# Performance work log

Measured on AMD Instinct MI355X. Metric: run time of the kernel, lower is better.

## Reference

```python
import jax, jax.numpy as jnp
import numpy as np


def setup_inputs() -> dict:
    key = jax.random.key(0)
    k1, k2, k3 = jax.random.split(key, 3)
    B, N, D = 4, 4096, 1024
    x = jax.random.normal(k1, (B, N, D), dtype=jnp.float32)
    # torch nn.Linear default init ~ U(-1/sqrt(D), 1/sqrt(D)); scale normals similarly
    scale = 1.0 / np.sqrt(D)
    Wq = jax.random.normal(k2, (D, D), dtype=jnp.float32) * scale
    Wk = jax.random.normal(k3, (D, D), dtype=jnp.float32) * scale
    return {"x": x, "Wq": Wq, "Wk": Wk}


def reference(x, Wq, Wk):
    # torch Linear: y = x @ W.T (weight shape [out, in])
    D = x.shape[-1]
    q = jnp.einsum('bnd,ed->bne', x, Wq)  # [B,N,D]
    k = jnp.einsum('bnd,ed->bne', x, Wk)  # [B,N,D]
    scores = jnp.einsum('bqd,bkd->bqk', q, k) / jnp.sqrt(jnp.float32(D))
    attn = jax.nn.softmax(scores, axis=-1)  # [B,N,N]
    return jnp.einsum('bqk,bkd->bqd', attn, x)
```

## Files before the change

### kernel.cpp

```cpp
#include <hip/hip_runtime.h>
#include <stdint.h>
#include <math.h>

typedef __attribute__((ext_vector_type(8))) short short8;
typedef __attribute__((ext_vector_type(4))) float fx4;
typedef unsigned int u32;

#define MFMA16(a, b, c) __builtin_amdgcn_mfma_f32_16x16x32_bf16(a, b, c, 0, 0, 0)
#define SCL 0.04508422002777948f

__device__ __forceinline__ unsigned short f2bfu(float f) {
  unsigned u = __builtin_bit_cast(unsigned, f);
  u += 0x7fffu + ((u >> 16) & 1u);
  return (unsigned short)(u >> 16);
}

__device__ __forceinline__ void gl_lds16(const void* g, void* l) {
  __builtin_amdgcn_global_load_lds(
      (const __attribute__((address_space(1))) u32*)g,
      (__attribute__((address_space(3))) u32*)l, 16, 0, 0);
}

__global__ __launch_bounds__(256) void prep_kernel(const float* __restrict__ x,
                                                   unsigned short* __restrict__ xT,
                                                   unsigned short* __restrict__ xbf) {
  __shared__ float tile[64 * 65];
  const int b = blockIdx.z, n0 = blockIdx.x * 64, d0 = blockIdx.y * 64;
  const int tid = threadIdx.x;
  const float* xb = x + ((size_t)b * 4096 + n0) * 1024 + d0;
#pragma unroll
  for (int i = 0; i < 4; i++) {
    int idx = tid + 256 * i;
    int r = idx >> 4, c4 = (idx & 15) * 4;
    const float4 v = *(const float4*)(xb + (size_t)r * 1024 + c4);
    float* tp = &tile[r * 65 + c4];
    tp[0] = v.x; tp[1] = v.y; tp[2] = v.z; tp[3] = v.w;
    uint2 pkt;
    pkt.x = (u32)f2bfu(v.x) | ((u32)f2bfu(v.y) << 16);
    pkt.y = (u32)f2bfu(v.z) | ((u32)f2bfu(v.w) << 16);
    *(uint2*)(xbf + ((size_t)b * 4096 + n0 + r) * 1024 + d0 + c4) = pkt;
  }
  __syncthreads();
  unsigned short* xo = xT + ((size_t)b * 1024 + d0) * 4096 + n0;
#pragma unroll
  for (int i = 0; i < 4; i++) {
    int idx = tid + 256 * i;
    int dr = idx >> 4, n4 = (idx & 15) * 4;
    unsigned short h0 = f2bfu(tile[(n4 + 0) * 65 + dr]);
    unsigned short h1 = f2bfu(tile[(n4 + 1) * 65 + dr]);
    unsigned short h2 = f2bfu(tile[(n4 + 2) * 65 + dr]);
    unsigned short h3 = f2bfu(tile[(n4 + 3) * 65 + dr]);
    uint2 pkt;
    pkt.x = (u32)h0 | ((u32)h1 << 16);
    pkt.y = (u32)h2 | ((u32)h3 << 16);
    *(uint2*)(xo + (size_t)dr * 4096 + n4) = pkt;
  }
}

__global__ __launch_bounds__(256) void wconv_kernel(const float* __restrict__ Wq,
                                                    const float* __restrict__ Wk,
                                                    unsigned short* __restrict__ Wqb,
                                                    unsigned short* __restrict__ Wkb) {
  int gid = blockIdx.x * 256 + threadIdx.x;
  const float* s = (gid < 262144) ? Wq : Wk;
  unsigned short* d = (gid < 262144) ? Wqb : Wkb;
  int off = (gid & 262143) * 4;
  const float4 v = *(const float4*)(s + off);
  uint2 pkt;
  pkt.x = (u32)f2bfu(v.x) | ((u32)f2bfu(v.y) << 16);
  pkt.y = (u32)f2bfu(v.z) | ((u32)f2bfu(v.w) << 16);
  *(uint2*)(d + off) = pkt;
}


__global__ __launch_bounds__(256) void proj_kernel(
    const unsigned short* __restrict__ xbf, const unsigned short* __restrict__ Wqb,
    const unsigned short* __restrict__ Wkb, unsigned short* __restrict__ Qo,
    unsigned short* __restrict__ Ko) {
  const unsigned short* Wb = blockIdx.z ? Wkb : Wqb;
  unsigned short* O = blockIdx.z ? Ko : Qo;
  __shared__ __attribute__((aligned(16))) short Als[128 * 64];
  __shared__ __attribute__((aligned(16))) short Bls[128 * 64];
  const int m0 = blockIdx.x * 128, e0 = blockIdx.y * 128;
  const int tid = threadIdx.x;
  const int wave = tid >> 6, lane = tid & 63;
  const int wm = wave & 1, wn = wave >> 1;
  const int quad = lane >> 4, l16 = lane & 15;

  const unsigned short* ag[4];
  const unsigned short* bg[4];
  short* al[4];
  short* bl[4];
#pragma unroll
  for (int i = 0; i < 4; i++) {
    const int s = tid + 256 * i;
    const int row = s >> 3, o = (s & 7) ^ (row & 7);
    ag[i] = xbf + (size_t)(m0 + row) * 1024 + o * 8;
    bg[i] = Wb + (size_t)(e0 + row) * 1024 + o * 8;
    al[i] = Als + s * 8;
    bl[i] = Bls + s * 8;
  }
  int aoff[4][2], boff[4][2];
#pragma unroll
  for (int t = 0; t < 4; t++)
#pragma unroll
    for (int st = 0; st < 2; st++) {
      const int ra = 64 * wm + 16 * t + l16;
      const int rb = 64 * wn + 16 * t + l16;
      aoff[t][st] = ra * 64 + (((st * 4 + quad) ^ (ra & 7)) * 8);
      boff[t][st] = rb * 64 + (((st * 4 + quad) ^ (rb & 7)) * 8);
    }

  fx4 acc[4][4];
#pragma unroll
  for (int i = 0; i < 4; i++)
#pragma unroll
    for (int j = 0; j < 4; j++) acc[i][j] = (fx4)0.f;

  for (int k0 = 0; k0 < 1024; k0 += 64) {
#pragma unroll
    for (int i = 0; i < 4; i++) {
      gl_lds16(ag[i] + k0, al[i]);
      gl_lds16(bg[i] + k0, bl[i]);
    }
    __syncthreads();
#pragma unroll
    for (int st = 0; st < 2; st++) {
      short8 af[4], bfv[4];
#pragma unroll
      for (int t = 0; t < 4; t++) {
        af[t] = *(const short8*)&Als[aoff[t][st]];
        bfv[t] = *(const short8*)&Bls[boff[t][st]];
      }
#pragma unroll
      for (int mt = 0; mt < 4; mt++)
#pragma unroll
        for (int nt = 0; nt < 4; nt++)
          acc[mt][nt] = MFMA16(af[mt], bfv[nt], acc[mt][nt]);
    }
    __syncthreads();
  }
#pragma unroll
  for (int mt = 0; mt < 4; mt++) {
    const int row = m0 + 64 * wm + 16 * mt + 4 * quad;
#pragma unroll
    for (int nt = 0; nt < 4; nt++) {
      const int col = e0 + 64 * wn + 16 * nt + l16;
      unsigned short* op = O + (size_t)row * 1024 + col;
#pragma unroll
      for (int i = 0; i < 4; i++) op[(size_t)i * 1024] = f2bfu(acc[mt][nt][i]);
    }
  }
}

__global__ __launch_bounds__(256) void qk_kernel(
    const unsigned short* __restrict__ Qb, const unsigned short* __restrict__ Kb,
    unsigned short* __restrict__ P, int bbase) {
  const int bz = blockIdx.z, b = bbase + bz;
  const unsigned short* A = Qb + (size_t)b * 4096 * 1024;
  const unsigned short* B = Kb + (size_t)b * 4096 * 1024;
  unsigned short* Pb = P + (size_t)bz * 4096 * 4096;
  __shared__ __attribute__((aligned(16))) short Als[128 * 64];
  __shared__ __attribute__((aligned(16))) short Bls[128 * 64];
  const int m0 = blockIdx.x * 128, n0 = blockIdx.y * 128;
  const int tid = threadIdx.x;
  const int wave = tid >> 6, lane = tid & 63;
  const int wm = wave & 1, wn = wave >> 1;
  const int quad = lane >> 4, l16 = lane & 15;

  const unsigned short* ag[4];
  const unsigned short* bg[4];
  short* al[4];
  short* bl[4];
#pragma unroll
  for (int i = 0; i < 4; i++) {
    const int s = tid + 256 * i;
    const int row = s >> 3, o = (s & 7) ^ (row & 7);
    ag[i] = A + (size_t)(m0 + row) * 1024 + o * 8;
    bg[i] = B + (size_t)(n0 + row) * 1024 + o * 8;
    al[i] = Als + s * 8;
    bl[i] = Bls + s * 8;
  }
  int aoff[4][2], boff[4][2];
#pragma unroll
  for (int t = 0; t < 4; t++)
#pragma unroll
    for (int st = 0; st < 2; st++) {
      const int ra = 64 * wm + 16 * t + l16;
      const int rb = 64 * wn + 16 * t + l16;
      aoff[t][st] = ra * 64 + (((st * 4 + quad) ^ (ra & 7)) * 8);
      boff[t][st] = rb * 64 + (((st * 4 + quad) ^ (rb & 7)) * 8);
    }

  fx4 acc[4][4];
#pragma unroll
  for (int i = 0; i < 4; i++)
#pragma unroll
    for (int j = 0; j < 4; j++) acc[i][j] = (fx4)0.f;

  for (int k0 = 0; k0 < 1024; k0 += 64) {
#pragma unroll
    for (int i = 0; i < 4; i++) {
      gl_lds16(ag[i] + k0, al[i]);
      gl_lds16(bg[i] + k0, bl[i]);
    }
    __syncthreads();
#pragma unroll
    for (int st = 0; st < 2; st++) {
      short8 af[4], bfv[4];
#pragma unroll
      for (int t = 0; t < 4; t++) {
        af[t] = *(const short8*)&Als[aoff[t][st]];
        bfv[t] = *(const short8*)&Bls[boff[t][st]];
      }
#pragma unroll
      for (int mt = 0; mt < 4; mt++)
#pragma unroll
        for (int nt = 0; nt < 4; nt++)
          acc[mt][nt] = MFMA16(af[mt], bfv[nt], acc[mt][nt]);
    }
    __syncthreads();
  }
#pragma unroll
  for (int mt = 0; mt < 4; mt++) {
    const int row = m0 + 64 * wm + 16 * mt + 4 * quad;
#pragma unroll
    for (int nt = 0; nt < 4; nt++) {
      const int col = n0 + 64 * wn + 16 * nt + l16;
      unsigned short* pp = Pb + (size_t)row * 4096 + col;
#pragma unroll
      for (int i = 0; i < 4; i++)
        pp[(size_t)i * 4096] = f2bfu(exp2f(acc[mt][nt][i] * SCL));
    }
  }
}

__global__ __launch_bounds__(256) void pv_kernel(
    const unsigned short* __restrict__ P, const unsigned short* __restrict__ xT,
    unsigned short* __restrict__ Ost, int bbase) {
  const int bz = blockIdx.z, b = bbase + bz;
  const unsigned short* A = P + (size_t)bz * 4096 * 4096;
  const unsigned short* B = xT + (size_t)b * 1024 * 4096;
  unsigned short* O = Ost + (size_t)b * 4096 * 1024;
  __shared__ __attribute__((aligned(16))) short Als[128 * 64];
  __shared__ __attribute__((aligned(16))) short Bls[128 * 64];
  const int m0 = blockIdx.x * 128, e0 = blockIdx.y * 128;
  const int tid = threadIdx.x;
  const int wave = tid >> 6, lane = tid & 63;
  const int wm = wave & 1, wn = wave >> 1;
  const int quad = lane >> 4, l16 = lane & 15;

  const unsigned short* ag[4];
  const unsigned short* bg[4];
  short* al[4];
  short* bl[4];
#pragma unroll
  for (int i = 0; i < 4; i++) {
    const int s = tid + 256 * i;
    const int row = s >> 3, o = (s & 7) ^ (row & 7);
    ag[i] = A + (size_t)(m0 + row) * 4096 + o * 8;
    bg[i] = B + (size_t)(e0 + row) * 4096 + o * 8;
    al[i] = Als + s * 8;
    bl[i] = Bls + s * 8;
  }
  int aoff[4][2], boff[4][2];
#pragma unroll
  for (int t = 0; t < 4; t++)
#pragma unroll
    for (int st = 0; st < 2; st++) {
      const int ra = 64 * wm + 16 * t + l16;
      const int rb = 64 * wn + 16 * t + l16;
      aoff[t][st] = ra * 64 + (((st * 4 + quad) ^ (ra & 7)) * 8);
      boff[t][st] = rb * 64 + (((st * 4 + quad) ^ (rb & 7)) * 8);
    }

  short8 ones;
#pragma unroll
  for (int i = 0; i < 8; i++) ones[i] = (short)0x3F80;

  fx4 acc[4][4], accl[4];
#pragma unroll
  for (int i = 0; i < 4; i++) {
    accl[i] = (fx4)0.f;
#pragma unroll
    for (int j = 0; j < 4; j++) acc[i][j] = (fx4)0.f;
  }

  for (int k0 = 0; k0 < 4096; k0 += 64) {
#pragma unroll
    for (int i = 0; i < 4; i++) {
      gl_lds16(ag[i] + k0, al[i]);
      gl_lds16(bg[i] + k0, bl[i]);
    }
    __syncthreads();
#pragma unroll
    for (int st = 0; st < 2; st++) {
      short8 af[4], bfv[4];
#pragma unroll
      for (int t = 0; t < 4; t++) {
        af[t] = *(const short8*)&Als[aoff[t][st]];
        bfv[t] = *(const short8*)&Bls[boff[t][st]];
      }
#pragma unroll
      for (int mt = 0; mt < 4; mt++) {
#pragma unroll
        for (int nt = 0; nt < 4; nt++)
          acc[mt][nt] = MFMA16(af[mt], bfv[nt], acc[mt][nt]);
        accl[mt] = MFMA16(af[mt], ones, accl[mt]);
      }
    }
    __syncthreads();
  }
#pragma unroll
  for (int mt = 0; mt < 4; mt++) {
    const int row = m0 + 64 * wm + 16 * mt + 4 * quad;
    const fx4 li = accl[mt];
#pragma unroll
    for (int nt = 0; nt < 4; nt++) {
      const int col = e0 + 64 * wn + 16 * nt + l16;
      unsigned short* op = O + (size_t)row * 1024 + col;
#pragma unroll
      for (int i = 0; i < 4; i++) op[(size_t)i * 1024] = f2bfu(acc[mt][nt][i] / li[i]);
    }
  }
}

__global__ __launch_bounds__(256) void fin_kernel(const uint4* __restrict__ Ost,
                                                  float4* __restrict__ out) {
  size_t t = (size_t)blockIdx.x * 256 + threadIdx.x;
  const uint4 v = Ost[t];
  float4 o0, o1;
  o0.x = __builtin_bit_cast(float, v.x << 16);
  o0.y = __builtin_bit_cast(float, v.x & 0xffff0000u);
  o0.z = __builtin_bit_cast(float, v.y << 16);
  o0.w = __builtin_bit_cast(float, v.y & 0xffff0000u);
  o1.x = __builtin_bit_cast(float, v.z << 16);
  o1.y = __builtin_bit_cast(float, v.z & 0xffff0000u);
  o1.z = __builtin_bit_cast(float, v.w << 16);
  o1.w = __builtin_bit_cast(float, v.w & 0xffff0000u);
  out[t * 2] = o0;
  out[t * 2 + 1] = o1;
}

extern "C" void kernel_launch(void* const* d_in, const int* in_sizes, int n_in,
                              void* d_out, int out_size, void* d_ws, size_t ws_size,
                              hipStream_t stream) {
  const float* x = (const float*)d_in[0];
  const float* Wq = (const float*)d_in[1];
  const float* Wk = (const float*)d_in[2];
  char* ws = (char*)d_ws;
  unsigned short* xT = (unsigned short*)ws;
  unsigned short* Qb = (unsigned short*)(ws + (size_t)33554432);
  unsigned short* Kb = (unsigned short*)(ws + (size_t)67108864);
  unsigned short* Ost = Qb;
  unsigned short* xbf = (unsigned short*)d_out;
  unsigned short* Wqb = (unsigned short*)((char*)d_out + (size_t)33554432);
  unsigned short* Wkb = (unsigned short*)((char*)d_out + (size_t)35651584);
  unsigned short* Pp = (unsigned short*)d_out;

  hipLaunchKernelGGL(prep_kernel, dim3(64, 16, 4), dim3(256), 0, stream, x, xT, xbf);
  hipLaunchKernelGGL(wconv_kernel, dim3(2048), dim3(256), 0, stream, Wq, Wk, Wqb, Wkb);
  hipLaunchKernelGGL(proj_kernel, dim3(128, 8, 2), dim3(256), 0, stream, xbf, Wqb, Wkb, Qb, Kb);
  hipLaunchKernelGGL(qk_kernel, dim3(32, 32, 2), dim3(256), 0, stream, Qb, Kb, Pp, 0);
  hipLaunchKernelGGL(pv_kernel, dim3(32, 8, 2), dim3(256), 0, stream, Pp, xT, Ost, 0);
  hipLaunchKernelGGL(qk_kernel, dim3(32, 32, 2), dim3(256), 0, stream, Qb, Kb, Pp, 2);
  hipLaunchKernelGGL(pv_kernel, dim3(32, 8, 2), dim3(256), 0, stream, Pp, xT, Ost, 2);
  hipLaunchKernelGGL(fin_kernel, dim3(8192), dim3(256), 0, stream,
                     (const uint4*)Ost, (float4*)d_out);
}
```

Before: 566.0 us.

## Rewrite GEMM kernels with 512-thread larger tiles and double-buffered staged pipeline

Replaces the simple single-buffered 128x128 GEMM loops in proj, qk and pv with 8-wave blocks using larger tiles (256x128, and 256x256 for qk). Global-to-LDS loads are double-buffered and issued in quarter-tile stages that interleave with MFMA phases, using explicit vmcnt waits, raw barriers and setprio. The aim is to hide global-load latency and increase operand reuse per LDS byte. The cost is more LDS per block (96KB and 128KB), lower occupancy and fragile hand-scheduled synchronisation.

```diff
diff --git a/kernel.cpp b/kernel.cpp
--- a/kernel.cpp
+++ b/kernel.cpp
@@ -8,6 +8,8 @@
 
 #define MFMA16(a, b, c) __builtin_amdgcn_mfma_f32_16x16x32_bf16(a, b, c, 0, 0, 0)
 #define SCL 0.04508422002777948f
+
+#define CFENCE asm volatile("" ::: "memory")
 
 __device__ __forceinline__ unsigned short f2bfu(float f) {
   unsigned u = __builtin_bit_cast(unsigned, f);
@@ -19,6 +21,12 @@
   __builtin_amdgcn_global_load_lds(
       (const __attribute__((address_space(1))) u32*)g,
       (__attribute__((address_space(3))) u32*)l, 16, 0, 0);
+}
+
+__device__ __forceinline__ void barx() {
+  CFENCE;
+  __builtin_amdgcn_s_barrier();
+  CFENCE;
 }
 
 __global__ __launch_bounds__(256) void prep_kernel(const float* __restrict__ x,
@@ -73,254 +81,335 @@
 }
 
 
-__global__ __launch_bounds__(256) void proj_kernel(
+template <int ONES, int NT, int LDA, int LDB>
+__device__ __forceinline__ void core128(const unsigned short* __restrict__ Ab,
+                                        const unsigned short* __restrict__ Bb,
+                                        short* lds, fx4 (&acc)[4][4], fx4 (&accl)[4]) {
+  constexpr int BUFB = 49152;
+  const int tid = threadIdx.x;
+  const int wave = tid >> 6, lane = tid & 63;
+  const int wm = wave >> 1, wn = wave & 1;
+  const int quad = lane >> 4, l16 = lane & 15;
+  char* lp = (char*)lds;
+
+  const int sr0 = tid >> 3, so0 = (tid & 7) ^ (sr0 & 7);
+  const int ga0 = sr0 * LDA + so0 * 8;
+  const int ga1 = ga0 + 64 * LDA;
+  const int gb0 = sr0 * LDB + so0 * 8;
+  const int ld0 = tid * 16;
+
+  const int cst0 = (quad ^ (l16 & 7)) * 16;
+  const int cst1 = ((4 + quad) ^ (l16 & 7)) * 16;
+  const int arb = (wm >> 1) * 16384 + (wm & 1) * 8192 + l16 * 128;
+  const int brb = 32768 + wn * 8192 + l16 * 128;
+
+  short8 ones;
+#pragma unroll
+  for (int i = 0; i < 8; i++) ones[i] = (short)0x3F80;
+#pragma unroll
+  for (int i = 0; i < 4; i++) {
+    accl[i] = (fx4)0.f;
+#pragma unroll
+    for (int j = 0; j < 4; j++) acc[i][j] = (fx4)0.f;
+  }
+
+#define PV_STGA(halfb, rowadd, bufb, kte)                                          \
+  do {                                                                             \
+    gl_lds16(Ab + (size_t)(rowadd) * LDA + (kte) + ga0, lp + (bufb) + (halfb) + ld0); \
+    gl_lds16(Ab + (size_t)(rowadd) * LDA + (kte) + ga1,                            \
+             lp + (bufb) + (halfb) + ld0 + 8192);                                  \
+  } while (0)
+#define PV_STGB(halfb, rowadd, bufb, kte) \
+  gl_lds16(Bb + (size_t)(rowadd) * LDB + (kte) + gb0, lp + (bufb) + 32768 + (halfb) + ld0)
+
+  PV_STGB(0, 0, 0, 0);
+  PV_STGA(0, 0, 0, 0);
+  PV_STGA(16384, 128, 0, 0);
+  PV_STGB(8192, 64, 0, 0);
+  PV_STGB(0, 0, BUFB, 64);
+  PV_STGA(0, 0, BUFB, 64);
+  asm volatile("s_waitcnt vmcnt(3)" ::: "memory");
+  barx();
+
+  short8 af[4], bf0[4], bf1[4];
+  for (int t = 0; t < NT; ++t) {
+    const int cbo = (t & 1) * BUFB, nbo = cbo ^ BUFB;
+    const int kt1 = ((t + 1) & (NT - 1)) * 64;
+    const int kt2 = ((t + 2) & (NT - 1)) * 64;
+#pragma unroll
+    for (int mt = 0; mt < 2; mt++) {
+      af[2 * mt] = *(const short8*)(lp + cbo + arb + mt * 2048 + cst0);
+      af[2 * mt + 1] = *(const short8*)(lp + cbo + arb + mt * 2048 + cst1);
+    }
+#pragma unroll
+    for (int nt = 0; nt < 2; nt++) {
+      bf0[2 * nt] = *(const short8*)(lp + cbo + brb + nt * 2048 + cst0);
+      bf0[2 * nt + 1] = *(const short8*)(lp + cbo + brb + nt * 2048 + cst1);
+    }
+    PV_STGA(16384, 128, nbo, kt1);
+    barx();
+    __builtin_amdgcn_s_setprio(1);
+#pragma unroll
+    for (int mt = 0; mt < 2; mt++) {
+#pragma unroll
+      for (int nt = 0; nt < 2; nt++) {
+        acc[mt][nt] = MFMA16(af[2 * mt], bf0[2 * nt], acc[mt][nt]);
+        acc[mt][nt] = MFMA16(af[2 * mt + 1], bf0[2 * nt + 1], acc[mt][nt]);
+      }
+      if (ONES) {
+        accl[mt] = MFMA16(af[2 * mt], ones, accl[mt]);
+        accl[mt] = MFMA16(af[2 * mt + 1], ones, accl[mt]);
+      }
+    }
+    __builtin_amdgcn_s_setprio(0);
+    barx();
+#pragma unroll
+    for (int nt = 0; nt < 2; nt++) {
+      bf1[2 * nt] = *(const short8*)(lp + cbo + brb + (nt + 2) * 2048 + cst0);
+      bf1[2 * nt + 1] = *(const short8*)(lp + cbo + brb + (nt + 2) * 2048 + cst1);
+    }
+    PV_STGB(8192, 64, nbo, kt1);
+    barx();
+    __builtin_amdgcn_s_setprio(1);
+#pragma unroll
+    for (int mt = 0; mt < 2; mt++)
+#pragma unroll
+      for (int nt = 0; nt < 2; nt++) {
+        acc[mt][nt + 2] = MFMA16(af[2 * mt], bf1[2 * nt], acc[mt][nt + 2]);
+        acc[mt][nt + 2] = MFMA16(af[2 * mt + 1], bf1[2 * nt + 1], acc[mt][nt + 2]);
+      }
+    __builtin_amdgcn_s_setprio(0);
+    barx();
+#pragma unroll
+    for (int mt = 0; mt < 2; mt++) {
+      af[2 * mt] = *(const short8*)(lp + cbo + arb + (mt + 2) * 2048 + cst0);
+      af[2 * mt + 1] = *(const short8*)(lp + cbo + arb + (mt + 2) * 2048 + cst1);
+    }
+    PV_STGB(0, 0, cbo, kt2);
+    barx();
+    __builtin_amdgcn_s_setprio(1);
+#pragma unroll
+    for (int mt = 0; mt < 2; mt++) {
+#pragma unroll
+      for (int nt = 0; nt < 2; nt++) {
+        acc[mt + 2][nt + 2] = MFMA16(af[2 * mt], bf1[2 * nt], acc[mt + 2][nt + 2]);
+        acc[mt + 2][nt + 2] = MFMA16(af[2 * mt + 1], bf1[2 * nt + 1], acc[mt + 2][nt + 2]);
+      }
+      if (ONES) {
+        accl[mt + 2] = MFMA16(af[2 * mt], ones, accl[mt + 2]);
+        accl[mt + 2] = MFMA16(af[2 * mt + 1], ones, accl[mt + 2]);
+      }
+    }
+    __builtin_amdgcn_s_setprio(0);
+    barx();
+    PV_STGA(0, 0, cbo, kt2);
+    asm volatile("s_waitcnt vmcnt(3)" ::: "memory");
+    barx();
+    __builtin_amdgcn_s_setprio(1);
+#pragma unroll
+    for (int mt = 0; mt < 2; mt++)
+#pragma unroll
+      for (int nt = 0; nt < 2; nt++) {
+        acc[mt + 2][nt] = MFMA16(af[2 * mt], bf0[2 * nt], acc[mt + 2][nt]);
+        acc[mt + 2][nt] = MFMA16(af[2 * mt + 1], bf0[2 * nt + 1], acc[mt + 2][nt]);
+      }
+    __builtin_amdgcn_s_setprio(0);
+    barx();
+  }
+#undef PV_STGA
+#undef PV_STGB
+}
+
+__global__ __launch_bounds__(512) void proj_kernel(
     const unsigned short* __restrict__ xbf, const unsigned short* __restrict__ Wqb,
     const unsigned short* __restrict__ Wkb, unsigned short* __restrict__ Qo,
     unsigned short* __restrict__ Ko) {
+  __shared__ __attribute__((aligned(16))) short lds[49152];
   const unsigned short* Wb = blockIdx.z ? Wkb : Wqb;
   unsigned short* O = blockIdx.z ? Ko : Qo;
-  __shared__ __attribute__((aligned(16))) short Als[128 * 64];
-  __shared__ __attribute__((aligned(16))) short Bls[128 * 64];
-  const int m0 = blockIdx.x * 128, e0 = blockIdx.y * 128;
+  const int m0 = blockIdx.x * 256, e0 = blockIdx.y * 128;
+  fx4 acc[4][4], accl[4];
+  core128<0, 16, 1024, 1024>(xbf + (size_t)m0 * 1024, Wb + (size_t)e0 * 1024, lds, acc, accl);
+  const int wave = threadIdx.x >> 6, lane = threadIdx.x & 63;
+  const int wm = wave >> 1, wn = wave & 1;
+  const int quad = lane >> 4, l16 = lane & 15;
+#pragma unroll
+  for (int mt = 0; mt < 4; mt++) {
+    const int row = m0 + wm * 64 + mt * 16 + quad * 4;
+#pragma unroll
+    for (int nt = 0; nt < 4; nt++) {
+      const int col = e0 + wn * 64 + nt * 16 + l16;
+      unsigned short* op = O + (size_t)row * 1024 + col;
+#pragma unroll
+      for (int i = 0; i < 4; i++) op[(size_t)i * 1024] = f2bfu(acc[mt][nt][i]);
+    }
+  }
+}
+
+__global__ __launch_bounds__(512) void pv_kernel(
+    const unsigned short* __restrict__ P, const unsigned short* __restrict__ xT,
+    unsigned short* __restrict__ Ost, int bbase) {
+  __shared__ __attribute__((aligned(16))) short lds[49152];
+  const int bz = blockIdx.z, b = bbase + bz;
+  const int m0 = blockIdx.x * 256, e0 = blockIdx.y * 128;
+  const unsigned short* Ab = P + (size_t)bz * 4096 * 4096 + (size_t)m0 * 4096;
+  const unsigned short* Bb = xT + (size_t)b * 1024 * 4096 + (size_t)e0 * 4096;
+  fx4 acc[4][4], accl[4];
+  core128<1, 64, 4096, 4096>(Ab, Bb, lds, acc, accl);
+  unsigned short* O = Ost + (size_t)b * 4096 * 1024;
+  const int wave = threadIdx.x >> 6, lane = threadIdx.x & 63;
+  const int wm = wave >> 1, wn = wave & 1;
+  const int quad = lane >> 4, l16 = lane & 15;
+#pragma unroll
+  for (int mt = 0; mt < 4; mt++) {
+    const int row = m0 + wm * 64 + mt * 16 + quad * 4;
+    const fx4 li = accl[mt];
+#pragma unroll
+    for (int nt = 0; nt < 4; nt++) {
+      const int col = e0 + wn * 64 + nt * 16 + l16;
+      unsigned short* op = O + (size_t)row * 1024 + col;
+#pragma unroll
+      for (int i = 0; i < 4; i++) op[(size_t)i * 1024] = f2bfu(acc[mt][nt][i] / li[i]);
+    }
+  }
+}
+
+__global__ __launch_bounds__(512) void qk_kernel(
+    const unsigned short* __restrict__ Qb, const unsigned short* __restrict__ Kb,
+    unsigned short* __restrict__ Pp, int bbase) {
+  constexpr int NT = 16;
+  __shared__ __attribute__((aligned(16))) short lds[65536];
+  const int bz = blockIdx.z, b = bbase + bz;
+  const unsigned short* A = Qb + (size_t)b * 4096 * 1024;
+  const unsigned short* Bm = Kb + (size_t)b * 4096 * 1024;
+  unsigned short* Pb = Pp + (size_t)bz * 4096 * 4096;
+  const int m0 = blockIdx.x * 256, n0 = blockIdx.y * 256;
   const int tid = threadIdx.x;
   const int wave = tid >> 6, lane = tid & 63;
-  const int wm = wave & 1, wn = wave >> 1;
+  const int wm = wave >> 2, wn = wave & 3;
   const int quad = lane >> 4, l16 = lane & 15;
-
-  const unsigned short* ag[4];
-  const unsigned short* bg[4];
-  short* al[4];
-  short* bl[4];
-#pragma unroll
-  for (int i = 0; i < 4; i++) {
-    const int s = tid + 256 * i;
-    const int row = s >> 3, o = (s & 7) ^ (row & 7);
-    ag[i] = xbf + (size_t)(m0 + row) * 1024 + o * 8;
-    bg[i] = Wb + (size_t)(e0 + row) * 1024 + o * 8;
-    al[i] = Als + s * 8;
-    bl[i] = Bls + s * 8;
-  }
-  int aoff[4][2], boff[4][2];
-#pragma unroll
-  for (int t = 0; t < 4; t++)
-#pragma unroll
-    for (int st = 0; st < 2; st++) {
-      const int ra = 64 * wm + 16 * t + l16;
-      const int rb = 64 * wn + 16 * t + l16;
-      aoff[t][st] = ra * 64 + (((st * 4 + quad) ^ (ra & 7)) * 8);
-      boff[t][st] = rb * 64 + (((st * 4 + quad) ^ (rb & 7)) * 8);
-    }
-
-  fx4 acc[4][4];
-#pragma unroll
-  for (int i = 0; i < 4; i++)
+  char* lp = (char*)lds;
+
+  const unsigned short* Ab = A + (size_t)m0 * 1024;
+  const unsigned short* Bb = Bm + (size_t)n0 * 1024;
+  const int sr0 = tid >> 3, so0 = (tid & 7) ^ (sr0 & 7);
+  const int ga0 = sr0 * 1024 + so0 * 8;
+  const int ga1 = ga0 + 64 * 1024;
+  const int ld0 = tid * 16;
+
+  const int cst0 = (quad ^ (l16 & 7)) * 16;
+  const int cst1 = ((4 + quad) ^ (l16 & 7)) * 16;
+  const int arb = wm * 16384 + l16 * 128;
+  const int brb = 32768 + (wn >> 1) * 16384 + (wn & 1) * 8192 + l16 * 128;
+
+  fx4 acc[8][4];
+#pragma unroll
+  for (int i = 0; i < 8; i++)
 #pragma unroll
     for (int j = 0; j < 4; j++) acc[i][j] = (fx4)0.f;
 
-  for (int k0 = 0; k0 < 1024; k0 += 64) {
-#pragma unroll
-    for (int i = 0; i < 4; i++) {
-      gl_lds16(ag[i] + k0, al[i]);
-      gl_lds16(bg[i] + k0, bl[i]);
-    }
-    __syncthreads();
-#pragma unroll
-    for (int st = 0; st < 2; st++) {
-      short8 af[4], bfv[4];
-#pragma unroll
-      for (int t = 0; t < 4; t++) {
-        af[t] = *(const short8*)&Als[aoff[t][st]];
-        bfv[t] = *(const short8*)&Bls[boff[t][st]];
-      }
-#pragma unroll
-      for (int mt = 0; mt < 4; mt++)
-#pragma unroll
-        for (int nt = 0; nt < 4; nt++)
-          acc[mt][nt] = MFMA16(af[mt], bfv[nt], acc[mt][nt]);
-    }
-    __syncthreads();
-  }
-#pragma unroll
-  for (int mt = 0; mt < 4; mt++) {
-    const int row = m0 + 64 * wm + 16 * mt + 4 * quad;
+#define QK_STG(OPb, halfb, rowadd, bufb, kte)                                       \
+  do {                                                                              \
+    gl_lds16(OPb + (size_t)(rowadd) * 1024 + (kte) + ga0, lp + (bufb) + (halfb) + ld0); \
+    gl_lds16(OPb + (size_t)(rowadd) * 1024 + (kte) + ga1,                           \
+             lp + (bufb) + (halfb) + ld0 + 8192);                                   \
+  } while (0)
+
+  QK_STG(Bb, 32768, 0, 0, 0);
+  QK_STG(Ab, 0, 0, 0, 0);
+  QK_STG(Ab, 16384, 128, 0, 0);
+  QK_STG(Bb, 49152, 128, 0, 0);
+  QK_STG(Bb, 32768, 0, 65536, 64);
+  QK_STG(Ab, 0, 0, 65536, 64);
+  asm volatile("s_waitcnt vmcnt(4)" ::: "memory");
+  barx();
+
+  short8 af[8], bf0[4], bf1[4];
+  for (int t = 0; t < NT; ++t) {
+    const int cbo = (t & 1) * 65536, nbo = cbo ^ 65536;
+    const int kt1 = ((t + 1) & (NT - 1)) * 64;
+    const int kt2 = ((t + 2) & (NT - 1)) * 64;
+#pragma unroll
+    for (int mt = 0; mt < 4; mt++) {
+      af[2 * mt] = *(const short8*)(lp + cbo + arb + mt * 2048 + cst0);
+      af[2 * mt + 1] = *(const short8*)(lp + cbo + arb + mt * 2048 + cst1);
+    }
+#pragma unroll
+    for (int nt = 0; nt < 2; nt++) {
+      bf0[2 * nt] = *(const short8*)(lp + cbo + brb + nt * 2048 + cst0);
+      bf0[2 * nt + 1] = *(const short8*)(lp + cbo + brb + nt * 2048 + cst1);
+    }
+    QK_STG(Ab, 16384, 128, nbo, kt1);
+    barx();
+    __builtin_amdgcn_s_setprio(1);
+#pragma unroll
+    for (int mt = 0; mt < 4; mt++)
+#pragma unroll
+      for (int nt = 0; nt < 2; nt++) {
+        acc[mt][nt] = MFMA16(af[2 * mt], bf0[2 * nt], acc[mt][nt]);
+        acc[mt][nt] = MFMA16(af[2 * mt + 1], bf0[2 * nt + 1], acc[mt][nt]);
+      }
+    __builtin_amdgcn_s_setprio(0);
+    barx();
+#pragma unroll
+    for (int nt = 0; nt < 2; nt++) {
+      bf1[2 * nt] = *(const short8*)(lp + cbo + brb + (nt + 2) * 2048 + cst0);
+      bf1[2 * nt + 1] = *(const short8*)(lp + cbo + brb + (nt + 2) * 2048 + cst1);
+    }
+    QK_STG(Bb, 49152, 128, nbo, kt1);
+    barx();
+    __builtin_amdgcn_s_setprio(1);
+#pragma unroll
+    for (int mt = 0; mt < 4; mt++)
+#pragma unroll
+      for (int nt = 0; nt < 2; nt++) {
+        acc[mt][nt + 2] = MFMA16(af[2 * mt], bf1[2 * nt], acc[mt][nt + 2]);
+        acc[mt][nt + 2] = MFMA16(af[2 * mt + 1], bf1[2 * nt + 1], acc[mt][nt + 2]);
+      }
+    __builtin_amdgcn_s_setprio(0);
+    barx();
+#pragma unroll
+    for (int mt = 0; mt < 4; mt++) {
+      af[2 * mt] = *(const short8*)(lp + cbo + arb + (mt + 4) * 2048 + cst0);
+      af[2 * mt + 1] = *(const short8*)(lp + cbo + arb + (mt + 4) * 2048 + cst1);
+    }
+    QK_STG(Bb, 32768, 0, cbo, kt2);
+    barx();
+    __builtin_amdgcn_s_setprio(1);
+#pragma unroll
+    for (int mt = 0; mt < 4; mt++)
+#pragma unroll
+      for (int nt = 0; nt < 2; nt++) {
+        acc[mt + 4][nt + 2] = MFMA16(af[2 * mt], bf1[2 * nt], acc[mt + 4][nt + 2]);
+        acc[mt + 4][nt + 2] = MFMA16(af[2 * mt + 1], bf1[2 * nt + 1], acc[mt + 4][nt + 2]);
+      }
+    __builtin_amdgcn_s_setprio(0);
+    barx();
+    QK_STG(Ab, 0, 0, cbo, kt2);
+    asm volatile("s_waitcnt vmcnt(4)" ::: "memory");
+    barx();
+    __builtin_amdgcn_s_setprio(1);
+#pragma unroll
+    for (int mt = 0; mt < 4; mt++)
+#pragma unroll
+      for (int nt = 0; nt < 2; nt++) {
+        acc[mt + 4][nt] = MFMA16(af[2 * mt], bf0[2 * nt], acc[mt + 4][nt]);
+        acc[mt + 4][nt] = MFMA16(af[2 * mt + 1], bf0[2 * nt + 1], acc[mt + 4][nt]);
+      }
+    __builtin_amdgcn_s_setprio(0);
+    barx();
+  }
+#undef QK_STG
+#pragma unroll
+  for (int mt = 0; mt < 8; mt++) {
+    const int row = m0 + wm * 128 + mt * 16 + quad * 4;
 #pragma unroll
     for (int nt = 0; nt < 4; nt++) {
-      const int col = e0 + 64 * wn + 16 * nt + l16;
-      unsigned short* op = O + (size_t)row * 1024 + col;
-#pragma unroll
-      for (int i = 0; i < 4; i++) op[(size_t)i * 1024] = f2bfu(acc[mt][nt][i]);
-    }
-  }
-}
-
-__global__ __launch_bounds__(256) void qk_kernel(
-    const unsigned short* __restrict__ Qb, const unsigned short* __restrict__ Kb,
-    unsigned short* __restrict__ P, int bbase) {
-  const int bz = blockIdx.z, b = bbase + bz;
-  const unsigned short* A = Qb + (size_t)b * 4096 * 1024;
-  const unsigned short* B = Kb + (size_t)b * 4096 * 1024;
-  unsigned short* Pb = P + (size_t)bz * 4096 * 4096;
-  __shared__ __attribute__((aligned(16))) short Als[128 * 64];
-  __shared__ __attribute__((aligned(16))) short Bls[128 * 64];
-  const int m0 = blockIdx.x * 128, n0 = blockIdx.y * 128;
-  const int tid = threadIdx.x;
-  const int wave = tid >> 6, lane = tid & 63;
-  const int wm = wave & 1, wn = wave >> 1;
-  const int quad = lane >> 4, l16 = lane & 15;
-
-  const unsigned short* ag[4];
-  const unsigned short* bg[4];
-  short* al[4];
-  short* bl[4];
-#pragma unroll
-  for (int i = 0; i < 4; i++) {
-    const int s = tid + 256 * i;
-    const int row = s >> 3, o = (s & 7) ^ (row & 7);
-    ag[i] = A + (size_t)(m0 + row) * 1024 + o * 8;
-    bg[i] = B + (size_t)(n0 + row) * 1024 + o * 8;
-    al[i] = Als + s * 8;
-    bl[i] = Bls + s * 8;
-  }
-  int aoff[4][2], boff[4][2];
-#pragma unroll
-  for (int t = 0; t < 4; t++)
-#pragma unroll
-    for (int st = 0; st < 2; st++) {
-      const int ra = 64 * wm + 16 * t + l16;
-      const int rb = 64 * wn + 16 * t + l16;
-      aoff[t][st] = ra * 64 + (((st * 4 + quad) ^ (ra & 7)) * 8);
-      boff[t][st] = rb * 64 + (((st * 4 + quad) ^ (rb & 7)) * 8);
-    }
-
-  fx4 acc[4][4];
-#pragma unroll
-  for (int i = 0; i < 4; i++)
-#pragma unroll
-    for (int j = 0; j < 4; j++) acc[i][j] = (fx4)0.f;
-
-  for (int k0 = 0; k0 < 1024; k0 += 64) {
-#pragma unroll
-    for (int i = 0; i < 4; i++) {
-      gl_lds16(ag[i] + k0, al[i]);
-      gl_lds16(bg[i] + k0, bl[i]);
-    }
-    __syncthreads();
-#pragma unroll
-    for (int st = 0; st < 2; st++) {
-      short8 af[4], bfv[4];
-#pragma unroll
-      for (int t = 0; t < 4; t++) {
-        af[t] = *(const short8*)&Als[aoff[t][st]];
-        bfv[t] = *(const short8*)&Bls[boff[t][st]];
-      }
-#pragma unroll
-      for (int mt = 0; mt < 4; mt++)
-#pragma unroll
-        for (int nt = 0; nt < 4; nt++)
-          acc[mt][nt] = MFMA16(af[mt], bfv[nt], acc[mt][nt]);
-    }
-    __syncthreads();
-  }
-#pragma unroll
-  for (int mt = 0; mt < 4; mt++) {
-    const int row = m0 + 64 * wm + 16 * mt + 4 * quad;
-#pragma unroll
-    for (int nt = 0; nt < 4; nt++) {
-      const int col = n0 + 64 * wn + 16 * nt + l16;
+      const int col = n0 + wn * 64 + nt * 16 + l16;
       unsigned short* pp = Pb + (size_t)row * 4096 + col;
 #pragma unroll
       for (int i = 0; i < 4; i++)
         pp[(size_t)i * 4096] = f2bfu(exp2f(acc[mt][nt][i] * SCL));
-    }
-  }
-}
-
-__global__ __launch_bounds__(256) void pv_kernel(
-    const unsigned short* __restrict__ P, const unsigned short* __restrict__ xT,
-    unsigned short* __restrict__ Ost, int bbase) {
-  const int bz = blockIdx.z, b = bbase + bz;
-  const unsigned short* A = P + (size_t)bz * 4096 * 4096;
-  const unsigned short* B = xT + (size_t)b * 1024 * 4096;
-  unsigned short* O = Ost + (size_t)b * 4096 * 1024;
-  __shared__ __attribute__((aligned(16))) short Als[128 * 64];
-  __shared__ __attribute__((aligned(16))) short Bls[128 * 64];
-  const int m0 = blockIdx.x * 128, e0 = blockIdx.y * 128;
-  const int tid = threadIdx.x;
-  const int wave = tid >> 6, lane = tid & 63;
-  const int wm = wave & 1, wn = wave >> 1;
-  const int quad = lane >> 4, l16 = lane & 15;
-
-  const unsigned short* ag[4];
-  const unsigned short* bg[4];
-  short* al[4];
-  short* bl[4];
-#pragma unroll
-  for (int i = 0; i < 4; i++) {
-    const int s = tid + 256 * i;
-    const int row = s >> 3, o = (s & 7) ^ (row & 7);
-    ag[i] = A + (size_t)(m0 + row) * 4096 + o * 8;
-    bg[i] = B + (size_t)(e0 + row) * 4096 + o * 8;
-    al[i] = Als + s * 8;
-    bl[i] = Bls + s * 8;
-  }
-  int aoff[4][2], boff[4][2];
-#pragma unroll
-  for (int t = 0; t < 4; t++)
-#pragma unroll
-    for (int st = 0; st < 2; st++) {
-      const int ra = 64 * wm + 16 * t + l16;
-      const int rb = 64 * wn + 16 * t + l16;
-      aoff[t][st] = ra * 64 + (((st * 4 + quad) ^ (ra & 7)) * 8);
-      boff[t][st] = rb * 64 + (((st * 4 + quad) ^ (rb & 7)) * 8);
-    }
-
-  short8 ones;
-#pragma unroll
-  for (int i = 0; i < 8; i++) ones[i] = (short)0x3F80;
-
-  fx4 acc[4][4], accl[4];
-#pragma unroll
-  for (int i = 0; i < 4; i++) {
-    accl[i] = (fx4)0.f;
-#pragma unroll
-    for (int j = 0; j < 4; j++) acc[i][j] = (fx4)0.f;
-  }
-
-  for (int k0 = 0; k0 < 4096; k0 += 64) {
-#pragma unroll
-    for (int i = 0; i < 4; i++) {
-      gl_lds16(ag[i] + k0, al[i]);
-      gl_lds16(bg[i] + k0, bl[i]);
-    }
-    __syncthreads();
-#pragma unroll
-    for (int st = 0; st < 2; st++) {
-      short8 af[4], bfv[4];
-#pragma unroll
-      for (int t = 0; t < 4; t++) {
-        af[t] = *(const short8*)&Als[aoff[t][st]];
-        bfv[t] = *(const short8*)&Bls[boff[t][st]];
-      }
-#pragma unroll
-      for (int mt = 0; mt < 4; mt++) {
-#pragma unroll
-        for (int nt = 0; nt < 4; nt++)
-          acc[mt][nt] = MFMA16(af[mt], bfv[nt], acc[mt][nt]);
-        accl[mt] = MFMA16(af[mt], ones, accl[mt]);
-      }
-    }
-    __syncthreads();
-  }
-#pragma unroll
-  for (int mt = 0; mt < 4; mt++) {
-    const int row = m0 + 64 * wm + 16 * mt + 4 * quad;
-    const fx4 li = accl[mt];
-#pragma unroll
-    for (int nt = 0; nt < 4; nt++) {
-      const int col = e0 + 64 * wn + 16 * nt + l16;
-      unsigned short* op = O + (size_t)row * 1024 + col;
-#pragma unroll
-      for (int i = 0; i < 4; i++) op[(size_t)i * 1024] = f2bfu(acc[mt][nt][i] / li[i]);
     }
   }
 }
@@ -360,11 +449,11 @@
 
   hipLaunchKernelGGL(prep_kernel, dim3(64, 16, 4), dim3(256), 0, stream, x, xT, xbf);
   hipLaunchKernelGGL(wconv_kernel, dim3(2048), dim3(256), 0, stream, Wq, Wk, Wqb, Wkb);
-  hipLaunchKernelGGL(proj_kernel, dim3(128, 8, 2), dim3(256), 0, stream, xbf, Wqb, Wkb, Qb, Kb);
-  hipLaunchKernelGGL(qk_kernel, dim3(32, 32, 2), dim3(256), 0, stream, Qb, Kb, Pp, 0);
-  hipLaunchKernelGGL(pv_kernel, dim3(32, 8, 2), dim3(256), 0, stream, Pp, xT, Ost, 0);
-  hipLaunchKernelGGL(qk_kernel, dim3(32, 32, 2), dim3(256), 0, stream, Qb, Kb, Pp, 2);
-  hipLaunchKernelGGL(pv_kernel, dim3(32, 8, 2), dim3(256), 0, stream, Pp, xT, Ost, 2);
+  hipLaunchKernelGGL(proj_kernel, dim3(64, 8, 2), dim3(512), 0, stream, xbf, Wqb, Wkb, Qb, Kb);
+  hipLaunchKernelGGL(qk_kernel, dim3(16, 16, 2), dim3(512), 0, stream, Qb, Kb, Pp, 0);
+  hipLaunchKernelGGL(pv_kernel, dim3(16, 8, 2), dim3(512), 0, stream, Pp, xT, Ost, 0);
+  hipLaunchKernelGGL(qk_kernel, dim3(16, 16, 2), dim3(512), 0, stream, Qb, Kb, Pp, 2);
+  hipLaunchKernelGGL(pv_kernel, dim3(16, 8, 2), dim3(512), 0, stream, Pp, xT, Ost, 2);
   hipLaunchKernelGGL(fin_kernel, dim3(8192), dim3(256), 0, stream,
                      (const uint4*)Ost, (float4*)d_out);
 }
```

Measured after the change: 500.6 us. 11.6% less time.
